# Performance work log

Hardware: AMD Instinct MI355X
Metric: run time of the kernel (lower is better)

Reference implementation:

```python
import jax, jax.numpy as jnp
import numpy as np

D_MODEL, D_SLOT, D_HIDDEN = 256, 256, 128


def setup_inputs() -> dict:
    key = jax.random.key(0)
    k1, k2, k3, k4, k5, k6 = jax.random.split(key, 6)
    B, T, N = 8, 1024, 64
    features = jax.random.normal(k1, (B, T, D_MODEL), dtype=jnp.float32)
    slots = jax.random.normal(k2, (B, N, D_SLOT), dtype=jnp.float32)
    # nn.Linear-style init (uniform +- 1/sqrt(fan_in))
    lim1 = 1.0 / np.sqrt(D_MODEL + D_SLOT)
    W_proj = jax.random.uniform(k3, (D_MODEL + D_SLOT, D_HIDDEN), minval=-lim1, maxval=lim1, dtype=jnp.float32)
    b_proj = jax.random.uniform(k4, (D_HIDDEN,), minval=-lim1, maxval=lim1, dtype=jnp.float32)
    lim2 = 1.0 / np.sqrt(D_HIDDEN)
    w_head = jax.random.uniform(k5, (D_HIDDEN,), minval=-lim2, maxval=lim2, dtype=jnp.float32)
    b_head = jax.random.uniform(k6, (), minval=-lim2, maxval=lim2, dtype=jnp.float32)
    return {"features": features, "slots": slots, "W_proj": W_proj, "b_proj": b_proj, "w_head": w_head, "b_head": b_head}


def reference(features, slots, W_proj, b_proj, w_head, b_head):
    # proj(concat([feat, slot])) is separable: feat @ W_f + slot @ W_s + b
    W_f = W_proj[:D_MODEL]   # (D, H)
    W_s = W_proj[D_MODEL:]   # (S, H)
    f_proj = jnp.einsum('btd,dh->bth', features, W_f)          # (B, T, H)
    s_proj = jnp.einsum('bns,sh->bnh', slots, W_s) + b_proj    # (B, N, H)
    x = jax.nn.relu(f_proj[:, :, None, :] + s_proj[:, None, :, :])  # (B, T, N, H)
    out = jnp.einsum('btnh,h->btn', x, w_head) + b_head         # (B, T, N)
    return out
```

## Files before the change

kernel.cpp:

```cpp
#include <hip/hip_runtime.h>
#include <hip/hip_bf16.h>
#include <hip/hip_fp16.h>

typedef unsigned short ushort_t;
typedef unsigned int uint_t;
typedef __attribute__((ext_vector_type(8))) short short8;
typedef __attribute__((ext_vector_type(4))) float f32x4;
typedef __attribute__((ext_vector_type(4))) unsigned int uint4v;
typedef __attribute__((ext_vector_type(2))) _Float16 half2v;

#if defined(__has_builtin)
#if __has_builtin(__builtin_amdgcn_fdot2)
#define HAVE_FDOT2 1
#endif
#endif

__device__ __forceinline__ ushort_t f2bf(float f) {
    unsigned v;
    __builtin_memcpy(&v, &f, 4);
    unsigned r = (v + 0x7FFFu + ((v >> 16) & 1u)) >> 16;
    return (ushort_t)r;
}

__global__ __launch_bounds__(1024) void asd_k1(
        const float* __restrict__ slots,
        const float* __restrict__ Wproj,
        const float* __restrict__ bproj,
        ushort_t* __restrict__ s2,
        ushort_t* __restrict__ Wpack) {
    int bid = blockIdx.x;
    int tid = threadIdx.x;
    if (bid < 256) {
        __shared__ float sl[512];
        __shared__ float part[3][256];
        int b  = bid >> 5;
        int n0 = (bid & 31) * 2;
        const float* srow = slots + (b * 64 + n0) * 256;
        if (tid < 256) {
            float2 v = ((const float2*)srow)[tid];
            sl[2 * tid]     = v.x;
            sl[2 * tid + 1] = v.y;
        }
        __syncthreads();
        int dh = tid >> 8;
        int nl = (tid >> 7) & 1;
        int h  = tid & 127;
        const float* Wcol = Wproj + 256 * 128 + dh * 64 * 128 + h;
        const float* sr   = sl + nl * 256 + dh * 64;
        float acc = 0.f;
        #pragma unroll 8
        for (int d = 0; d < 64; ++d)
            acc += sr[d] * Wcol[d * 128];
        if (dh) part[dh - 1][nl * 128 + h] = acc;
        __syncthreads();
        if (dh == 0) {
            float v = acc + part[0][nl * 128 + h] + part[1][nl * 128 + h]
                          + part[2][nl * 128 + h] + bproj[h];
            _Float16 hv = (_Float16)v;
            ushort_t u;
            __builtin_memcpy(&u, &hv, 2);
            int n = n0 + nl;
            s2[b * 8192 + (h >> 1) * 128 + n * 2 + (h & 1)] = u;
        }
    } else {
        int gid = (bid - 256) * 1024 + tid;
        int l   = gid & 63;
        int idx = gid >> 6;
        int kb  = idx >> 3, nt = idx & 7;
        int r0  = kb * 32 + ((l >> 4) << 3);
        int c   = nt * 16 + (l & 15);
        short8 frag;
        #pragma unroll
        for (int i = 0; i < 8; ++i)
            frag[i] = (short)f2bf(Wproj[(r0 + i) * 128 + c]);
        ((short8*)Wpack)[gid] = frag;
    }
}

__global__ __launch_bounds__(256) void asd_k2(
        const float* __restrict__ feat,
        const ushort_t* __restrict__ s2g,
        const ushort_t* __restrict__ Wpack,
        const float* __restrict__ whead,
        const float* __restrict__ bhead,
        float* __restrict__ out) {
    __shared__ uint_t   s2_lds[64 * 68];
    __shared__ ushort_t f_lds[16 * 132];
    __shared__ uint_t   w2_lds[64];

    int tid = threadIdx.x;
    int bid = blockIdx.x;
    int b   = bid >> 6;
    int t0  = (bid & 63) << 4;

    if (tid < 64) {
        half2v w2 = { (_Float16)whead[2 * tid], (_Float16)whead[2 * tid + 1] };
        uint_t u;
        __builtin_memcpy(&u, &w2, 4);
        w2_lds[tid] = u;
    }
    const uint4v* src = (const uint4v*)(s2g + b * 8192);
    #pragma unroll
    for (int r = 0; r < 4; ++r) {
        int i4 = r * 256 + tid;
        int h2 = i4 >> 4, c = i4 & 15;
        *(uint4v*)(s2_lds + h2 * 68 + c * 4) = src[i4];
    }
    float bh = bhead[0];

    int l = tid & 63;
    int w = tid >> 6;
    int m = l & 15, q = l >> 4;
    int nt0 = 2 * w;
    f32x4 acc0 = {0.f, 0.f, 0.f, 0.f};
    f32x4 acc1 = {0.f, 0.f, 0.f, 0.f};
    const short8* Wp = (const short8*)Wpack;
    #pragma unroll
    for (int kb = 0; kb < 8; ++kb) {
        const float* arow = feat + (b * 1024 + t0 + m) * 256 + kb * 32 + q * 8;
        f32x4 af0 = *(const f32x4*)arow;
        f32x4 af1 = *(const f32x4*)(arow + 4);
        __hip_bfloat162 c0 = __float22bfloat162_rn(make_float2(af0[0], af0[1]));
        __hip_bfloat162 c1 = __float22bfloat162_rn(make_float2(af0[2], af0[3]));
        __hip_bfloat162 c2 = __float22bfloat162_rn(make_float2(af1[0], af1[1]));
        __hip_bfloat162 c3 = __float22bfloat162_rn(make_float2(af1[2], af1[3]));
        uint_t u0, u1, u2, u3;
        __builtin_memcpy(&u0, &c0, 4);
        __builtin_memcpy(&u1, &c1, 4);
        __builtin_memcpy(&u2, &c2, 4);
        __builtin_memcpy(&u3, &c3, 4);
        uint4v au = {u0, u1, u2, u3};
        short8 A;
        __builtin_memcpy(&A, &au, 16);
        short8 B0 = Wp[(kb * 8 + nt0) * 64 + l];
        short8 B1 = Wp[(kb * 8 + nt0 + 1) * 64 + l];
        acc0 = __builtin_amdgcn_mfma_f32_16x16x32_bf16(A, B0, acc0, 0, 0, 0);
        acc1 = __builtin_amdgcn_mfma_f32_16x16x32_bf16(A, B1, acc1, 0, 0, 0);
    }
    #pragma unroll
    for (int r = 0; r < 4; ++r) {
        int row = q * 4 + r;
        _Float16 v0 = (_Float16)acc0[r];
        _Float16 v1 = (_Float16)acc1[r];
        ushort_t u0, u1;
        __builtin_memcpy(&u0, &v0, 2);
        __builtin_memcpy(&u1, &v1, 2);
        f_lds[row * 132 + nt0 * 16 + m]       = u0;
        f_lds[row * 132 + (nt0 + 1) * 16 + m] = u1;
    }
    __syncthreads();

    int t = tid >> 4, ng = tid & 15;
    const ushort_t* fR = f_lds + t * 132;
    float a0 = bh, a1 = bh, a2 = bh, a3 = bh;
    const half2v hz = { (_Float16)0.f, (_Float16)0.f };
    #pragma unroll 8
    for (int h2 = 0; h2 < 64; ++h2) {
        uint_t fu = *(const uint_t*)(fR + 2 * h2);
        half2v f2;
        __builtin_memcpy(&f2, &fu, 4);
        uint4v s4 = *(const uint4v*)(s2_lds + h2 * 68 + 4 * ng);
        uint_t wu = w2_lds[h2];
        half2v w2;
        __builtin_memcpy(&w2, &wu, 4);
        float* accs[4] = {&a0, &a1, &a2, &a3};
        #pragma unroll
        for (int j = 0; j < 4; ++j) {
            uint_t su = s4[j];
            half2v sv;
            __builtin_memcpy(&sv, &su, 4);
            half2v x = f2 + sv;
            x = __builtin_elementwise_max(x, hz);
#ifdef HAVE_FDOT2
            *accs[j] = __builtin_amdgcn_fdot2(x, w2, *accs[j], false);
#else
            *accs[j] += (float)x[0] * (float)w2[0] + (float)x[1] * (float)w2[1];
#endif
        }
    }
    f32x4 o = {a0, a1, a2, a3};
    *(f32x4*)(out + (b * 1024 + t0 + t) * 64 + 4 * ng) = o;
}

extern "C" void kernel_launch(void* const* d_in, const int* in_sizes, int n_in,
                              void* d_out, int out_size, void* d_ws, size_t ws_size,
                              hipStream_t stream) {
    const float* feat  = (const float*)d_in[0];
    const float* slots = (const float*)d_in[1];
    const float* Wproj = (const float*)d_in[2];
    const float* bproj = (const float*)d_in[3];
    const float* whead = (const float*)d_in[4];
    const float* bhead = (const float*)d_in[5];
    float* out = (float*)d_out;

    ushort_t* s2    = (ushort_t*)d_ws;
    ushort_t* Wpack = (ushort_t*)((char*)d_ws + 131072);

    hipLaunchKernelGGL(asd_k1, dim3(260), dim3(1024), 0, stream,
                       slots, Wproj, bproj, s2, Wpack);
    hipLaunchKernelGGL(asd_k2, dim3(512), dim3(256), 0, stream,
                       feat, s2, Wpack, whead, bhead, out);
}
```

Measured before the change: 79.22 us.

## Fuse slot projection and scoring into one kernel with per-batch flag sync

```diff
diff --git a/kernel.cpp b/kernel.cpp
--- a/kernel.cpp
+++ b/kernel.cpp
@@ -9,6 +9,8 @@
 typedef __attribute__((ext_vector_type(4))) unsigned int uint4v;
 typedef __attribute__((ext_vector_type(2))) _Float16 half2v;
 
+#define FLAG_MAGIC 0x13579BDFu
+
 #if defined(__has_builtin)
 #if __has_builtin(__builtin_amdgcn_fdot2)
 #define HAVE_FDOT2 1
@@ -22,50 +24,61 @@
     return (ushort_t)r;
 }
 
-__global__ __launch_bounds__(1024) void asd_k1(
+__global__ __launch_bounds__(512, 2) void asd_fused(
+        const float* __restrict__ feat,
         const float* __restrict__ slots,
         const float* __restrict__ Wproj,
         const float* __restrict__ bproj,
+        const float* __restrict__ whead,
+        const float* __restrict__ bhead,
+        float* __restrict__ out,
         ushort_t* __restrict__ s2,
-        ushort_t* __restrict__ Wpack) {
+        ushort_t* __restrict__ wpackAll,
+        uint_t* __restrict__ flags) {
+    __shared__ float    sl[512];
+    __shared__ float    part[256];
+    __shared__ uint_t   s2_lds[64 * 68];
+    __shared__ ushort_t f_lds[32 * 132];
+    __shared__ uint_t   w2_lds[64];
+
+    int tid = threadIdx.x;
     int bid = blockIdx.x;
-    int tid = threadIdx.x;
-    if (bid < 256) {
-        __shared__ float sl[512];
-        __shared__ float part[3][256];
-        int b  = bid >> 5;
-        int n0 = (bid & 31) * 2;
-        const float* srow = slots + (b * 64 + n0) * 256;
-        if (tid < 256) {
-            float2 v = ((const float2*)srow)[tid];
-            sl[2 * tid]     = v.x;
-            sl[2 * tid + 1] = v.y;
-        }
-        __syncthreads();
+    int b   = bid >> 5;
+    int j2  = bid & 31;
+
+    int n0 = j2 * 2;
+    if (tid < 256) {
+        float2 v = ((const float2*)(slots + (b * 64 + n0) * 256))[tid];
+        sl[2 * tid]     = v.x;
+        sl[2 * tid + 1] = v.y;
+    }
+    __syncthreads();
+    {
         int dh = tid >> 8;
         int nl = (tid >> 7) & 1;
         int h  = tid & 127;
-        const float* Wcol = Wproj + 256 * 128 + dh * 64 * 128 + h;
-        const float* sr   = sl + nl * 256 + dh * 64;
+        const float* Wcol = Wproj + 256 * 128 + dh * 128 * 128 + h;
+        const float* sr   = sl + nl * 256 + dh * 128;
         float acc = 0.f;
-        #pragma unroll 8
-        for (int d = 0; d < 64; ++d)
+        #pragma unroll 16
+        for (int d = 0; d < 128; ++d)
             acc += sr[d] * Wcol[d * 128];
-        if (dh) part[dh - 1][nl * 128 + h] = acc;
+        if (dh) part[nl * 128 + h] = acc;
         __syncthreads();
-        if (dh == 0) {
-            float v = acc + part[0][nl * 128 + h] + part[1][nl * 128 + h]
-                          + part[2][nl * 128 + h] + bproj[h];
+        if (!dh) {
+            float v = acc + part[nl * 128 + h] + bproj[h];
             _Float16 hv = (_Float16)v;
             ushort_t u;
             __builtin_memcpy(&u, &hv, 2);
             int n = n0 + nl;
             s2[b * 8192 + (h >> 1) * 128 + n * 2 + (h & 1)] = u;
         }
-    } else {
-        int gid = (bid - 256) * 1024 + tid;
-        int l   = gid & 63;
-        int idx = gid >> 6;
+    }
+    ushort_t* wpb = wpackAll + b * 32768;
+    if (tid < 128) {
+        int f   = j2 * 128 + tid;
+        int l   = f & 63;
+        int idx = f >> 6;
         int kb  = idx >> 3, nt = idx & 7;
         int r0  = kb * 32 + ((l >> 4) << 3);
         int c   = nt * 16 + (l & 15);
@@ -73,84 +86,86 @@
         #pragma unroll
         for (int i = 0; i < 8; ++i)
             frag[i] = (short)f2bf(Wproj[(r0 + i) * 128 + c]);
-        ((short8*)Wpack)[gid] = frag;
-    }
-}
-
-__global__ __launch_bounds__(256) void asd_k2(
-        const float* __restrict__ feat,
-        const ushort_t* __restrict__ s2g,
-        const ushort_t* __restrict__ Wpack,
-        const float* __restrict__ whead,
-        const float* __restrict__ bhead,
-        float* __restrict__ out) {
-    __shared__ uint_t   s2_lds[64 * 68];
-    __shared__ ushort_t f_lds[16 * 132];
-    __shared__ uint_t   w2_lds[64];
-
-    int tid = threadIdx.x;
-    int bid = blockIdx.x;
-    int b   = bid >> 6;
-    int t0  = (bid & 63) << 4;
-
+        ((short8*)wpb)[f] = frag;
+    }
+    __threadfence();
+    __syncthreads();
+    if (tid == 0)
+        __hip_atomic_store(&flags[bid], FLAG_MAGIC, __ATOMIC_RELEASE,
+                           __HIP_MEMORY_SCOPE_AGENT);
+
+    if (tid < 32) {
+        while (__hip_atomic_load(&flags[b * 32 + tid], __ATOMIC_ACQUIRE,
+                                 __HIP_MEMORY_SCOPE_AGENT) != FLAG_MAGIC)
+            __builtin_amdgcn_s_sleep(2);
+    }
+    __threadfence();
+    __syncthreads();
+
+    const uint4v* src = (const uint4v*)(s2 + b * 8192);
+    #pragma unroll
+    for (int r = 0; r < 2; ++r) {
+        int i4 = r * 512 + tid;
+        int h2 = i4 >> 4, c = i4 & 15;
+        *(uint4v*)(s2_lds + h2 * 68 + c * 4) = src[i4];
+    }
     if (tid < 64) {
         half2v w2 = { (_Float16)whead[2 * tid], (_Float16)whead[2 * tid + 1] };
         uint_t u;
         __builtin_memcpy(&u, &w2, 4);
         w2_lds[tid] = u;
     }
-    const uint4v* src = (const uint4v*)(s2g + b * 8192);
-    #pragma unroll
-    for (int r = 0; r < 4; ++r) {
-        int i4 = r * 256 + tid;
-        int h2 = i4 >> 4, c = i4 & 15;
-        *(uint4v*)(s2_lds + h2 * 68 + c * 4) = src[i4];
-    }
     float bh = bhead[0];
 
-    int l = tid & 63;
-    int w = tid >> 6;
-    int m = l & 15, q = l >> 4;
-    int nt0 = 2 * w;
-    f32x4 acc0 = {0.f, 0.f, 0.f, 0.f};
-    f32x4 acc1 = {0.f, 0.f, 0.f, 0.f};
-    const short8* Wp = (const short8*)Wpack;
-    #pragma unroll
-    for (int kb = 0; kb < 8; ++kb) {
-        const float* arow = feat + (b * 1024 + t0 + m) * 256 + kb * 32 + q * 8;
-        f32x4 af0 = *(const f32x4*)arow;
-        f32x4 af1 = *(const f32x4*)(arow + 4);
-        __hip_bfloat162 c0 = __float22bfloat162_rn(make_float2(af0[0], af0[1]));
-        __hip_bfloat162 c1 = __float22bfloat162_rn(make_float2(af0[2], af0[3]));
-        __hip_bfloat162 c2 = __float22bfloat162_rn(make_float2(af1[0], af1[1]));
-        __hip_bfloat162 c3 = __float22bfloat162_rn(make_float2(af1[2], af1[3]));
-        uint_t u0, u1, u2, u3;
-        __builtin_memcpy(&u0, &c0, 4);
-        __builtin_memcpy(&u1, &c1, 4);
-        __builtin_memcpy(&u2, &c2, 4);
-        __builtin_memcpy(&u3, &c3, 4);
-        uint4v au = {u0, u1, u2, u3};
-        short8 A;
-        __builtin_memcpy(&A, &au, 16);
-        short8 B0 = Wp[(kb * 8 + nt0) * 64 + l];
-        short8 B1 = Wp[(kb * 8 + nt0 + 1) * 64 + l];
-        acc0 = __builtin_amdgcn_mfma_f32_16x16x32_bf16(A, B0, acc0, 0, 0, 0);
-        acc1 = __builtin_amdgcn_mfma_f32_16x16x32_bf16(A, B1, acc1, 0, 0, 0);
-    }
-    #pragma unroll
-    for (int r = 0; r < 4; ++r) {
-        int row = q * 4 + r;
-        _Float16 v0 = (_Float16)acc0[r];
-        _Float16 v1 = (_Float16)acc1[r];
-        ushort_t u0, u1;
-        __builtin_memcpy(&u0, &v0, 2);
-        __builtin_memcpy(&u1, &v1, 2);
-        f_lds[row * 132 + nt0 * 16 + m]       = u0;
-        f_lds[row * 132 + (nt0 + 1) * 16 + m] = u1;
-    }
-    __syncthreads();
-
-    int t = tid >> 4, ng = tid & 15;
+    int t0 = j2 * 32;
+    {
+        int w    = tid >> 6;
+        int l    = tid & 63;
+        int tile = w >> 2;
+        int nt0  = 2 * (w & 3);
+        int m = l & 15, q = l >> 4;
+        f32x4 acc0 = {0.f, 0.f, 0.f, 0.f};
+        f32x4 acc1 = {0.f, 0.f, 0.f, 0.f};
+        const short8* Wp = (const short8*)wpb;
+        #pragma unroll
+        for (int kb = 0; kb < 8; ++kb) {
+            const float* arow =
+                feat + (b * 1024 + t0 + tile * 16 + m) * 256 + kb * 32 + q * 8;
+            f32x4 af0 = *(const f32x4*)arow;
+            f32x4 af1 = *(const f32x4*)(arow + 4);
+            __hip_bfloat162 c0 = __float22bfloat162_rn(make_float2(af0[0], af0[1]));
+            __hip_bfloat162 c1 = __float22bfloat162_rn(make_float2(af0[2], af0[3]));
+            __hip_bfloat162 c2 = __float22bfloat162_rn(make_float2(af1[0], af1[1]));
+            __hip_bfloat162 c3 = __float22bfloat162_rn(make_float2(af1[2], af1[3]));
+            uint_t u0, u1, u2, u3;
+            __builtin_memcpy(&u0, &c0, 4);
+            __builtin_memcpy(&u1, &c1, 4);
+            __builtin_memcpy(&u2, &c2, 4);
+            __builtin_memcpy(&u3, &c3, 4);
+            uint4v au = {u0, u1, u2, u3};
+            short8 A;
+            __builtin_memcpy(&A, &au, 16);
+            short8 B0 = Wp[(kb * 8 + nt0) * 64 + l];
+            short8 B1 = Wp[(kb * 8 + nt0 + 1) * 64 + l];
+            acc0 = __builtin_amdgcn_mfma_f32_16x16x32_bf16(A, B0, acc0, 0, 0, 0);
+            acc1 = __builtin_amdgcn_mfma_f32_16x16x32_bf16(A, B1, acc1, 0, 0, 0);
+        }
+        #pragma unroll
+        for (int r = 0; r < 4; ++r) {
+            int row = tile * 16 + q * 4 + r;
+            _Float16 v0 = (_Float16)acc0[r];
+            _Float16 v1 = (_Float16)acc1[r];
+            ushort_t u0, u1;
+            __builtin_memcpy(&u0, &v0, 2);
+            __builtin_memcpy(&u1, &v1, 2);
+            f_lds[row * 132 + nt0 * 16 + m]       = u0;
+            f_lds[row * 132 + (nt0 + 1) * 16 + m] = u1;
+        }
+    }
+    __syncthreads();
+
+    int t  = tid >> 4;
+    int ng = tid & 15;
     const ushort_t* fR = f_lds + t * 132;
     float a0 = bh, a1 = bh, a2 = bh, a3 = bh;
     const half2v hz = { (_Float16)0.f, (_Float16)0.f };
@@ -193,11 +208,11 @@
     const float* bhead = (const float*)d_in[5];
     float* out = (float*)d_out;
 
-    ushort_t* s2    = (ushort_t*)d_ws;
-    ushort_t* Wpack = (ushort_t*)((char*)d_ws + 131072);
-
-    hipLaunchKernelGGL(asd_k1, dim3(260), dim3(1024), 0, stream,
-                       slots, Wproj, bproj, s2, Wpack);
-    hipLaunchKernelGGL(asd_k2, dim3(512), dim3(256), 0, stream,
-                       feat, s2, Wpack, whead, bhead, out);
+    ushort_t* s2       = (ushort_t*)d_ws;
+    ushort_t* wpackAll = (ushort_t*)((char*)d_ws + 131072);
+    uint_t*   flags    = (uint_t*)((char*)d_ws + 655360);
+
+    hipLaunchKernelGGL(asd_fused, dim3(256), dim3(512), 0, stream,
+                       feat, slots, Wproj, bproj, whead, bhead,
+                       out, s2, wpackAll, flags);
 }
```

Result: slower. 154.2 us (+94.6%).
